# Performance work log

Hardware: AMD Instinct MI355X
Metric: run time of the kernel (lower is better)

Reference implementation:

```python
import jax, jax.numpy as jnp
import numpy as np

N0, N1, N2 = 20000, 15000, 15000
N = N0 + N1 + N2            # total nodes
E = 800000                  # edges (avg degree 16)
H, C = 128, 64


def setup_inputs() -> dict:
    key = jax.random.key(0)
    ks = jax.random.split(key, 16)
    s = 0.05  # weight scale
    return {
        "feat0": jax.random.normal(ks[0], (N0, 512), jnp.float32),
        "feat1": jax.random.normal(ks[1], (N1, 256), jnp.float32),
        "feat2": jax.random.normal(ks[2], (N2, 128), jnp.float32),
        "W0": jax.random.normal(ks[3], (512, H), jnp.float32) * s,
        "b0": jnp.zeros((H,), jnp.float32),
        "W1": jax.random.normal(ks[4], (256, H), jnp.float32) * s,
        "b1": jnp.zeros((H,), jnp.float32),
        "W2": jax.random.normal(ks[5], (128, H), jnp.float32) * s,
        "b2": jnp.zeros((H,), jnp.float32),
        "bias_l0": jnp.zeros((H,), jnp.float32),
        "W_l1": jax.random.normal(ks[6], (H, H), jnp.float32) * s,
        "b_l1": jnp.zeros((H,), jnp.float32),
        "W_l2": jax.random.normal(ks[7], (H, C), jnp.float32) * s,
        "b_l2": jnp.zeros((C,), jnp.float32),
        "src": jax.random.randint(ks[8], (E,), 0, N, jnp.int32),
        "dst": jax.random.randint(ks[9], (E,), 0, N, jnp.int32),
    }


def _norms(src, dst):
    # DGL GraphConv norm='both': src side uses out-degree, dst side in-degree
    ones = jnp.ones((E,), jnp.float32)
    deg_out = jax.ops.segment_sum(ones, src, num_segments=N)
    deg_in = jax.ops.segment_sum(ones, dst, num_segments=N)
    return jnp.maximum(deg_out, 1.0) ** -0.5, jnp.maximum(deg_in, 1.0) ** -0.5


def _agg(h, src, dst, norm_src, norm_dst):
    # normalized sparse aggregation: D_in^{-1/2} A D_out^{-1/2} h
    m = (h * norm_src[:, None])[src]                     # [E, d] gather
    a = jax.ops.segment_sum(m, dst, num_segments=N)      # [N, d] scatter-add
    return a * norm_dst[:, None]


def reference(feat0, feat1, feat2, W0, b0, W1, b1, W2, b2,
              bias_l0, W_l1, b_l1, W_l2, b_l2, src, dst):
    # per-node-type linear projections, concatenated along node axis
    h = jnp.concatenate([feat0 @ W0 + b0,
                         feat1 @ W1 + b1,
                         feat2 @ W2 + b2], axis=0)       # [N, H]
    ns, nd = _norms(src, dst)
    # layer 0: GraphConv(weight=False) -> agg + bias + relu (dropout = eval identity)
    h = jax.nn.relu(_agg(h, src, dst, ns, nd) + bias_l0)
    # layer 1: agg + linear + relu
    h = jax.nn.relu(_agg(h, src, dst, ns, nd) @ W_l1 + b_l1)
    # layer 2: agg + linear (no activation)
    h = _agg(h, src, dst, ns, nd) @ W_l2 + b_l2          # [N, C]
    return h
```

## Files before the change

kernel.cpp:

```cpp
#include <hip/hip_runtime.h>
#include <hip/hip_fp16.h>

#define N_NODES 50000
#define N0_ 20000
#define N1_ 15000
#define N2_ 15000
#define E_EDGES 800000
#define H_ 128
#define C_ 64

#define PB0 ((N0_ + 63) / 64)
#define PB1 ((N1_ + 63) / 64)
#define PB2 ((N2_ + 63) / 64)
#define PB_TOTAL (PB0 + PB1 + PB2)
#define EB ((E_EDGES + 255) / 256)
#define SB ((N_NODES + 255) / 256)


template <int TN, bool BIAS, bool RELU, bool SCALE, typename OT>
__device__ __forceinline__ void gemm_block(
    const float* __restrict__ A, const float* __restrict__ W,
    const float* __restrict__ bias, const float* __restrict__ rowscale,
    OT* __restrict__ out, int M, int K, int m0, float* As, float* Bs) {
    constexpr int NJ = TN / 32;
    constexpr int TN4 = TN / 4;
    int tid = threadIdx.x;
    int tx = tid & 31;
    int ty = tid >> 5;

    float acc[8][NJ];
#pragma unroll
    for (int i = 0; i < 8; i++)
#pragma unroll
        for (int j = 0; j < NJ; j++) acc[i][j] = 0.f;

    for (int k0 = 0; k0 < K; k0 += 32) {
#pragma unroll
        for (int t0 = 0; t0 < 2; t0++) {
            int t = tid + t0 * 256;
            int row = t >> 3;
            int c = t & 7;
            float4 v = make_float4(0.f, 0.f, 0.f, 0.f);
            if (m0 + row < M) v = *reinterpret_cast<const float4*>(&A[(size_t)(m0 + row) * K + k0 + c * 4]);
            As[(c * 4 + 0) * 68 + row] = v.x;
            As[(c * 4 + 1) * 68 + row] = v.y;
            As[(c * 4 + 2) * 68 + row] = v.z;
            As[(c * 4 + 3) * 68 + row] = v.w;
        }
#pragma unroll
        for (int t0 = 0; t0 < 32 * TN4 / 256; t0++) {
            int t = tid + t0 * 256;
            int r = t / TN4;
            int c4 = t % TN4;
            *reinterpret_cast<float4*>(&Bs[r * TN + c4 * 4]) =
                *reinterpret_cast<const float4*>(&W[(size_t)(k0 + r) * TN + c4 * 4]);
        }
        __syncthreads();
#pragma unroll 8
        for (int k = 0; k < 32; k++) {
            float4 a0 = *reinterpret_cast<float4*>(&As[k * 68 + ty * 8]);
            float4 a1 = *reinterpret_cast<float4*>(&As[k * 68 + ty * 8 + 4]);
            float ar[8] = {a0.x, a0.y, a0.z, a0.w, a1.x, a1.y, a1.z, a1.w};
            float br[NJ];
#pragma unroll
            for (int j = 0; j < NJ; j++) br[j] = Bs[k * TN + tx + 32 * j];
#pragma unroll
            for (int i = 0; i < 8; i++)
#pragma unroll
                for (int j = 0; j < NJ; j++) acc[i][j] = fmaf(ar[i], br[j], acc[i][j]);
        }
        __syncthreads();
    }
#pragma unroll
    for (int i = 0; i < 8; i++) {
        int row = m0 + ty * 8 + i;
        if (row < M) {
            float sc = SCALE ? rowscale[row] : 1.f;
#pragma unroll
            for (int j = 0; j < NJ; j++) {
                float v = acc[i][j] + (BIAS ? bias[tx + 32 * j] : 0.f);
                if (RELU) v = fmaxf(v, 0.f);
                v *= sc;
                out[(size_t)row * TN + tx + 32 * j] = (OT)v;
            }
        }
    }
}


__global__ __launch_bounds__(256) void k1_proj_rank(
    const float* __restrict__ feat0, const float* __restrict__ feat1, const float* __restrict__ feat2,
    const float* __restrict__ W0, const float* __restrict__ b0,
    const float* __restrict__ W1, const float* __restrict__ b1,
    const float* __restrict__ W2, const float* __restrict__ b2,
    __half* __restrict__ h0h,
    const int* __restrict__ src, const int* __restrict__ dst,
    int* __restrict__ cnt, int* __restrict__ degO, int* __restrict__ rank) {
    __shared__ float As[32 * 68];
    __shared__ float Bs[32 * 128];
    int bid = blockIdx.x;
    if (bid < PB_TOTAL) {
        const float* A; const float* Wp; const float* bp; __half* op; int M, K, m0;
        if (bid < PB0) {
            A = feat0; Wp = W0; bp = b0; op = h0h; M = N0_; K = 512; m0 = bid * 64;
        } else if (bid < PB0 + PB1) {
            A = feat1; Wp = W1; bp = b1; op = h0h + (size_t)N0_ * H_; M = N1_; K = 256;
            m0 = (bid - PB0) * 64;
        } else {
            A = feat2; Wp = W2; bp = b2; op = h0h + (size_t)(N0_ + N1_) * H_; M = N2_; K = 128;
            m0 = (bid - PB0 - PB1) * 64;
        }
        gemm_block<128, true, false, false, __half>(A, Wp, bp, nullptr, op, M, K, m0, As, Bs);
    } else {
        int e = (bid - PB_TOTAL) * 256 + threadIdx.x;
        if (e < E_EDGES) {
            rank[e] = atomicAdd(&cnt[dst[e]], 1);
            atomicAdd(&degO[src[e]], 1);
        }
    }
}


__global__ __launch_bounds__(256) void scan1_kernel(
    const int* __restrict__ cnt, int* __restrict__ pre, int* __restrict__ blocksum) {
    __shared__ int buf[256];
    int t = threadIdx.x;
    int i = blockIdx.x * 256 + t;
    int tot = (i < N_NODES) ? cnt[i] : 0;
    buf[t] = tot;
    __syncthreads();
#pragma unroll
    for (int off = 1; off < 256; off <<= 1) {
        int v = (t >= off) ? buf[t - off] : 0;
        __syncthreads();
        buf[t] += v;
        __syncthreads();
    }
    if (i < N_NODES) pre[i] = buf[t] - tot;
    if (t == 255) blocksum[blockIdx.x] = buf[255];
}

__global__ __launch_bounds__(256) void scan2_kernel(
    const int* __restrict__ blocksum, int* __restrict__ blockoff, int* __restrict__ rowptr) {
    __shared__ int buf[256];
    int t = threadIdx.x;
    int v = (t < SB) ? blocksum[t] : 0;
    buf[t] = v;
    __syncthreads();
#pragma unroll
    for (int off = 1; off < 256; off <<= 1) {
        int u = (t >= off) ? buf[t - off] : 0;
        __syncthreads();
        buf[t] += u;
        __syncthreads();
    }
    if (t < SB) blockoff[t] = buf[t] - v;
    if (t == 255) rowptr[N_NODES] = buf[255];
}

__global__ __launch_bounds__(256) void scan3_kernel(
    const int* __restrict__ cnt, const int* __restrict__ degO, const int* __restrict__ pre,
    const int* __restrict__ blockoff, int* __restrict__ rowptr,
    float* __restrict__ ns, float* __restrict__ nd) {
    int i = blockIdx.x * 256 + threadIdx.x;
    if (i < N_NODES) {
        rowptr[i] = blockoff[blockIdx.x] + pre[i];
        ns[i] = rsqrtf(fmaxf((float)degO[i], 1.0f));
        nd[i] = rsqrtf(fmaxf((float)cnt[i], 1.0f));
    }
}


__global__ __launch_bounds__(256) void k2_fill(
    const int* __restrict__ src, const int* __restrict__ dst,
    const int* __restrict__ rowptr, const int* __restrict__ rank,
    int* __restrict__ col) {
    int e = blockIdx.x * 256 + threadIdx.x;
    if (e < E_EDGES) col[rowptr[dst[e]] + rank[e]] = src[e];
}


template <int CH, int NSLOAD, int EPI, int OUTH>
__global__ __launch_bounds__(256) void agg_h_kernel(
    const __half* __restrict__ h, const int* __restrict__ rowptr,
    const int* __restrict__ col, const float* __restrict__ ns,
    const float* __restrict__ nd, const float* __restrict__ bias,
    void* __restrict__ out) {
    constexpr int L = CH / 8;
    constexpr int EPW = 64 / L;
    int node = blockIdx.x * 4 + (threadIdx.x >> 6);
    if (node >= N_NODES) return;
    int lane = threadIdx.x & 63;
    int li = lane & (L - 1);
    int g = lane / L;
    const uint4* __restrict__ h8 = (const uint4*)h;
    int beg = rowptr[node], end = rowptr[node + 1];
    float a0[8] = {0.f, 0.f, 0.f, 0.f, 0.f, 0.f, 0.f, 0.f};
    float a1[8] = {0.f, 0.f, 0.f, 0.f, 0.f, 0.f, 0.f, 0.f};
    union U8 { uint4 u; __half2 h2[4]; };
    int e = beg + g;
    for (; e + EPW < end; e += 2 * EPW) {
        int s0 = col[e], s1 = col[e + EPW];
        U8 u0, u1;
        u0.u = h8[(size_t)s0 * L + li];
        u1.u = h8[(size_t)s1 * L + li];
        float w0 = NSLOAD ? ns[s0] : 1.f;
        float w1 = NSLOAD ? ns[s1] : 1.f;
#pragma unroll
        for (int p = 0; p < 4; p++) {
            float2 f0 = __half22float2(u0.h2[p]);
            float2 f1 = __half22float2(u1.h2[p]);
            if (NSLOAD) {
                a0[2 * p] = fmaf(w0, f0.x, a0[2 * p]);
                a0[2 * p + 1] = fmaf(w0, f0.y, a0[2 * p + 1]);
                a1[2 * p] = fmaf(w1, f1.x, a1[2 * p]);
                a1[2 * p + 1] = fmaf(w1, f1.y, a1[2 * p + 1]);
            } else {
                a0[2 * p] += f0.x;
                a0[2 * p + 1] += f0.y;
                a1[2 * p] += f1.x;
                a1[2 * p + 1] += f1.y;
            }
        }
    }
    if (e < end) {
        int s = col[e];
        U8 u0;
        u0.u = h8[(size_t)s * L + li];
        float w0 = NSLOAD ? ns[s] : 1.f;
#pragma unroll
        for (int p = 0; p < 4; p++) {
            float2 f0 = __half22float2(u0.h2[p]);
            if (NSLOAD) {
                a0[2 * p] = fmaf(w0, f0.x, a0[2 * p]);
                a0[2 * p + 1] = fmaf(w0, f0.y, a0[2 * p + 1]);
            } else {
                a0[2 * p] += f0.x;
                a0[2 * p + 1] += f0.y;
            }
        }
    }
#pragma unroll
    for (int j = 0; j < 8; j++) {
        float v = a0[j] + a1[j];
#pragma unroll
        for (int off = 32; off >= L; off >>= 1) v += __shfl_xor(v, off);
        a0[j] = v;
    }
    if (lane < L) {
        float w = nd[node];
#pragma unroll
        for (int j = 0; j < 8; j++) a0[j] *= w;
        if (EPI == 1) {
            float sc = ns[node];
#pragma unroll
            for (int j = 0; j < 8; j++)
                a0[j] = fmaxf(a0[j] + bias[li * 8 + j], 0.f) * sc;
        } else if (EPI == 2) {
#pragma unroll
            for (int j = 0; j < 8; j++) a0[j] += bias[li * 8 + j];
        }
        if (OUTH) {
            union { uint4 u; __half hh[8]; } cv;
#pragma unroll
            for (int j = 0; j < 8; j++) cv.hh[j] = __float2half(a0[j]);
            ((uint4*)out)[(size_t)node * L + li] = cv.u;
        } else {
            float4* o4 = (float4*)out;
            o4[(size_t)node * (CH / 4) + li * 2] = make_float4(a0[0], a0[1], a0[2], a0[3]);
            o4[(size_t)node * (CH / 4) + li * 2 + 1] = make_float4(a0[4], a0[5], a0[6], a0[7]);
        }
    }
}


template <int TN, bool BIAS, bool RELU, bool SCALE, typename OT>
__global__ __launch_bounds__(256) void gemm_kernel(
    const float* __restrict__ A, const float* __restrict__ W,
    const float* __restrict__ bias, const float* __restrict__ rowscale,
    OT* __restrict__ out, int M, int K) {
    __shared__ float As[32 * 68];
    __shared__ float Bs[32 * TN];
    gemm_block<TN, BIAS, RELU, SCALE, OT>(A, W, bias, rowscale, out, M, K, blockIdx.x * 64, As, Bs);
}


extern "C" void kernel_launch(void* const* d_in, const int* in_sizes, int n_in,
                              void* d_out, int out_size, void* d_ws, size_t ws_size,
                              hipStream_t stream) {
    const float* feat0 = (const float*)d_in[0];
    const float* feat1 = (const float*)d_in[1];
    const float* feat2 = (const float*)d_in[2];
    const float* W0 = (const float*)d_in[3];
    const float* b0 = (const float*)d_in[4];
    const float* W1 = (const float*)d_in[5];
    const float* b1 = (const float*)d_in[6];
    const float* W2 = (const float*)d_in[7];
    const float* b2 = (const float*)d_in[8];
    const float* bias_l0 = (const float*)d_in[9];
    const float* W_l1 = (const float*)d_in[10];
    const float* b_l1 = (const float*)d_in[11];
    const float* W_l2 = (const float*)d_in[12];
    const float* b_l2 = (const float*)d_in[13];
    const int* src = (const int*)d_in[14];
    const int* dst = (const int*)d_in[15];
    float* out = (float*)d_out;

    char* ws = (char*)d_ws;
    size_t off = 0;
    auto alloc = [&](size_t bytes) {
        size_t cur = off;
        off += (bytes + 255) & ~(size_t)255;
        return cur;
    };
    size_t hA_off = alloc((size_t)N_NODES * H_ * 4);
    size_t hB_off = alloc((size_t)N_NODES * H_ * 4);
    size_t h0h_off = alloc((size_t)N_NODES * H_ * 2);
    size_t h1h_off = alloc((size_t)N_NODES * H_ * 2);
    size_t h2h_off = alloc((size_t)N_NODES * C_ * 2);
    size_t cnt_off = alloc((size_t)N_NODES * 4);
    size_t degO_off = alloc((size_t)N_NODES * 4);
    size_t ns_off = alloc((size_t)N_NODES * 4);
    size_t nd_off = alloc((size_t)N_NODES * 4);
    size_t rowptr_off = alloc((size_t)(N_NODES + 1) * 4);
    size_t rank_off = alloc((size_t)E_EDGES * 4);
    size_t col_off = alloc((size_t)E_EDGES * 4);
    size_t pre_off = alloc((size_t)N_NODES * 4);
    size_t bsum_off = alloc((size_t)SB * 4);
    size_t boff_off = alloc((size_t)SB * 4);

    float* hA = (float*)(ws + hA_off);
    float* hB = (float*)(ws + hB_off);
    __half* h0h = (__half*)(ws + h0h_off);
    __half* h1h = (__half*)(ws + h1h_off);
    __half* h2h = (__half*)(ws + h2h_off);
    int* cnt = (int*)(ws + cnt_off);
    int* degO = (int*)(ws + degO_off);
    float* ns = (float*)(ws + ns_off);
    float* nd = (float*)(ws + nd_off);
    int* rowptr = (int*)(ws + rowptr_off);
    int* rank = (int*)(ws + rank_off);
    int* col = (int*)(ws + col_off);
    int* pre = (int*)(ws + pre_off);
    int* bsum = (int*)(ws + bsum_off);
    int* boff = (int*)(ws + boff_off);

    hipMemsetAsync(ws + cnt_off, 0, ns_off - cnt_off, stream);

    k1_proj_rank<<<PB_TOTAL + EB, 256, 0, stream>>>(
        feat0, feat1, feat2, W0, b0, W1, b1, W2, b2, h0h, src, dst, cnt, degO, rank);
    scan1_kernel<<<SB, 256, 0, stream>>>(cnt, pre, bsum);
    scan2_kernel<<<1, 256, 0, stream>>>(bsum, boff, rowptr);
    scan3_kernel<<<SB, 256, 0, stream>>>(cnt, degO, pre, boff, rowptr, ns, nd);
    k2_fill<<<EB, 256, 0, stream>>>(src, dst, rowptr, rank, col);

    const int AGB = (N_NODES + 3) / 4;
    agg_h_kernel<128, 1, 1, 1><<<AGB, 256, 0, stream>>>(h0h, rowptr, col, ns, nd, bias_l0, h1h);
    agg_h_kernel<128, 0, 0, 0><<<AGB, 256, 0, stream>>>(h1h, rowptr, col, ns, nd, nullptr, hA);
    gemm_kernel<128, true, true, true, float><<<(N_NODES + 63) / 64, 256, 0, stream>>>(
        hA, W_l1, b_l1, ns, hB, N_NODES, 128);
    gemm_kernel<64, false, false, false, __half><<<(N_NODES + 63) / 64, 256, 0, stream>>>(
        hB, W_l2, nullptr, nullptr, h2h, N_NODES, 128);
    agg_h_kernel<64, 0, 2, 0><<<AGB, 256, 0, stream>>>(h2h, rowptr, col, ns, nd, b_l2, out);
}
```

Measured before the change: 258.0 us.

## Switch GEMMs to packed fp16 dot2 with pre-packed weights and fp16 intermediates

```diff
diff --git a/kernel.cpp b/kernel.cpp
--- a/kernel.cpp
+++ b/kernel.cpp
@@ -16,14 +16,80 @@
 #define EB ((E_EDGES + 255) / 256)
 #define SB ((N_NODES + 255) / 256)
 
-
-template <int TN, bool BIAS, bool RELU, bool SCALE, typename OT>
-__device__ __forceinline__ void gemm_block(
-    const float* __restrict__ A, const float* __restrict__ W,
+#define WT2_0 0
+#define WT2_1 32768
+#define WT2_2 49152
+#define WT2_L1 57344
+#define WT2_L2 65536
+#define WT2_TOTAL 69632
+
+typedef _Float16 h2_t __attribute__((ext_vector_type(2)));
+
+__device__ __forceinline__ float fdot2f(h2_t a, h2_t b, float c) {
+#if __has_builtin(__builtin_amdgcn_fdot2)
+    return __builtin_amdgcn_fdot2(a, b, c, false);
+#else
+    return fmaf((float)a[0], (float)b[0], fmaf((float)a[1], (float)b[1], c));
+#endif
+}
+
+
+__global__ __launch_bounds__(256) void wt2_kernel(
+    const float* __restrict__ W0, const float* __restrict__ W1, const float* __restrict__ W2,
+    const float* __restrict__ Wl1, const float* __restrict__ Wl2,
+    h2_t* __restrict__ Wt2) {
+    int t = blockIdx.x * 256 + threadIdx.x;
+    if (t >= WT2_TOTAL) return;
+    const float* W;
+    int rel, NW;
+    if (t < WT2_1) { W = W0; rel = t; NW = 128; }
+    else if (t < WT2_2) { W = W1; rel = t - WT2_1; NW = 128; }
+    else if (t < WT2_L1) { W = W2; rel = t - WT2_2; NW = 128; }
+    else if (t < WT2_L2) { W = Wl1; rel = t - WT2_L1; NW = 128; }
+    else { W = Wl2; rel = t - WT2_L2; NW = 64; }
+    int k2 = rel / NW;
+    int n = rel % NW;
+    h2_t p = {(_Float16)W[(size_t)(2 * k2) * NW + n], (_Float16)W[(size_t)(2 * k2 + 1) * NW + n]};
+    Wt2[t] = p;
+}
+
+
+__device__ __forceinline__ void stage_a_tile(const float* __restrict__ A, h2_t* As2,
+                                             int M, int K, int m0, int k0, int tid) {
+#pragma unroll
+    for (int t0 = 0; t0 < 2; t0++) {
+        int idx = tid + t0 * 256;
+        int row = idx >> 3;
+        int c = idx & 7;
+        float4 v = make_float4(0.f, 0.f, 0.f, 0.f);
+        if (m0 + row < M)
+            v = *reinterpret_cast<const float4*>(&A[(size_t)(m0 + row) * K + k0 + c * 4]);
+        h2_t p0 = {(_Float16)v.x, (_Float16)v.y};
+        h2_t p1 = {(_Float16)v.z, (_Float16)v.w};
+        As2[(c * 2) * 68 + row] = p0;
+        As2[(c * 2 + 1) * 68 + row] = p1;
+    }
+}
+
+__device__ __forceinline__ void stage_a_tile(const __half* __restrict__ A, h2_t* As2,
+                                             int M, int K, int m0, int k0, int tid) {
+    int row = tid >> 2;
+    int c = tid & 3;
+    union { uint4 u; h2_t p[4]; } v;
+    v.u = make_uint4(0, 0, 0, 0);
+    if (m0 + row < M)
+        v.u = *reinterpret_cast<const uint4*>(&A[(size_t)(m0 + row) * K + k0 + c * 8]);
+#pragma unroll
+    for (int i = 0; i < 4; i++) As2[(c * 4 + i) * 68 + row] = v.p[i];
+}
+
+
+template <int TN, bool BIAS, bool RELU, bool SCALE, typename IT, typename OT>
+__device__ __forceinline__ void gemm_block_h(
+    const IT* __restrict__ A, const h2_t* __restrict__ Wt2,
     const float* __restrict__ bias, const float* __restrict__ rowscale,
-    OT* __restrict__ out, int M, int K, int m0, float* As, float* Bs) {
+    OT* __restrict__ out, int M, int K, int m0, h2_t* As2, h2_t* Bs2) {
     constexpr int NJ = TN / 32;
-    constexpr int TN4 = TN / 4;
     int tid = threadIdx.x;
     int tx = tid & 31;
     int ty = tid >> 5;
@@ -35,39 +101,29 @@
         for (int j = 0; j < NJ; j++) acc[i][j] = 0.f;
 
     for (int k0 = 0; k0 < K; k0 += 32) {
-#pragma unroll
-        for (int t0 = 0; t0 < 2; t0++) {
-            int t = tid + t0 * 256;
-            int row = t >> 3;
-            int c = t & 7;
-            float4 v = make_float4(0.f, 0.f, 0.f, 0.f);
-            if (m0 + row < M) v = *reinterpret_cast<const float4*>(&A[(size_t)(m0 + row) * K + k0 + c * 4]);
-            As[(c * 4 + 0) * 68 + row] = v.x;
-            As[(c * 4 + 1) * 68 + row] = v.y;
-            As[(c * 4 + 2) * 68 + row] = v.z;
-            As[(c * 4 + 3) * 68 + row] = v.w;
-        }
-#pragma unroll
-        for (int t0 = 0; t0 < 32 * TN4 / 256; t0++) {
-            int t = tid + t0 * 256;
-            int r = t / TN4;
-            int c4 = t % TN4;
-            *reinterpret_cast<float4*>(&Bs[r * TN + c4 * 4]) =
-                *reinterpret_cast<const float4*>(&W[(size_t)(k0 + r) * TN + c4 * 4]);
-        }
-        __syncthreads();
-#pragma unroll 8
-        for (int k = 0; k < 32; k++) {
-            float4 a0 = *reinterpret_cast<float4*>(&As[k * 68 + ty * 8]);
-            float4 a1 = *reinterpret_cast<float4*>(&As[k * 68 + ty * 8 + 4]);
-            float ar[8] = {a0.x, a0.y, a0.z, a0.w, a1.x, a1.y, a1.z, a1.w};
-            float br[NJ];
-#pragma unroll
-            for (int j = 0; j < NJ; j++) br[j] = Bs[k * TN + tx + 32 * j];
+        stage_a_tile(A, As2, M, K, m0, k0, tid);
+        {
+            const uint4* g = reinterpret_cast<const uint4*>(Wt2 + (size_t)(k0 / 2) * TN);
+            uint4* l = reinterpret_cast<uint4*>(Bs2);
+            constexpr int CNT = 16 * TN / 4;
+#pragma unroll
+            for (int t0 = 0; t0 < CNT / 256; t0++) l[tid + t0 * 256] = g[tid + t0 * 256];
+        }
+        __syncthreads();
+#pragma unroll
+        for (int k2 = 0; k2 < 16; k2++) {
+            union { uint4 u; h2_t p[4]; } ua, ub;
+            ua.u = *reinterpret_cast<uint4*>(&As2[k2 * 68 + ty * 8]);
+            ub.u = *reinterpret_cast<uint4*>(&As2[k2 * 68 + ty * 8 + 4]);
+            h2_t ap[8] = {ua.p[0], ua.p[1], ua.p[2], ua.p[3],
+                          ub.p[0], ub.p[1], ub.p[2], ub.p[3]};
+            h2_t bp[NJ];
+#pragma unroll
+            for (int j = 0; j < NJ; j++) bp[j] = Bs2[k2 * TN + tx + 32 * j];
 #pragma unroll
             for (int i = 0; i < 8; i++)
 #pragma unroll
-                for (int j = 0; j < NJ; j++) acc[i][j] = fmaf(ar[i], br[j], acc[i][j]);
+                for (int j = 0; j < NJ; j++) acc[i][j] = fdot2f(ap[i], bp[j], acc[i][j]);
         }
         __syncthreads();
     }
@@ -90,27 +146,28 @@
 
 __global__ __launch_bounds__(256) void k1_proj_rank(
     const float* __restrict__ feat0, const float* __restrict__ feat1, const float* __restrict__ feat2,
-    const float* __restrict__ W0, const float* __restrict__ b0,
-    const float* __restrict__ W1, const float* __restrict__ b1,
-    const float* __restrict__ W2, const float* __restrict__ b2,
+    const h2_t* __restrict__ Wt2,
+    const float* __restrict__ b0, const float* __restrict__ b1, const float* __restrict__ b2,
     __half* __restrict__ h0h,
     const int* __restrict__ src, const int* __restrict__ dst,
     int* __restrict__ cnt, int* __restrict__ degO, int* __restrict__ rank) {
-    __shared__ float As[32 * 68];
-    __shared__ float Bs[32 * 128];
+    __shared__ h2_t As2[16 * 68];
+    __shared__ h2_t Bs2[16 * 128];
     int bid = blockIdx.x;
     if (bid < PB_TOTAL) {
-        const float* A; const float* Wp; const float* bp; __half* op; int M, K, m0;
+        const float* A; const float* bp; const h2_t* Wp; int M, K, m0;
+        size_t obase;
         if (bid < PB0) {
-            A = feat0; Wp = W0; bp = b0; op = h0h; M = N0_; K = 512; m0 = bid * 64;
+            A = feat0; bp = b0; Wp = Wt2 + WT2_0; M = N0_; K = 512; m0 = bid * 64; obase = 0;
         } else if (bid < PB0 + PB1) {
-            A = feat1; Wp = W1; bp = b1; op = h0h + (size_t)N0_ * H_; M = N1_; K = 256;
-            m0 = (bid - PB0) * 64;
+            A = feat1; bp = b1; Wp = Wt2 + WT2_1; M = N1_; K = 256; m0 = (bid - PB0) * 64;
+            obase = (size_t)N0_ * H_;
         } else {
-            A = feat2; Wp = W2; bp = b2; op = h0h + (size_t)(N0_ + N1_) * H_; M = N2_; K = 128;
-            m0 = (bid - PB0 - PB1) * 64;
-        }
-        gemm_block<128, true, false, false, __half>(A, Wp, bp, nullptr, op, M, K, m0, As, Bs);
+            A = feat2; bp = b2; Wp = Wt2 + WT2_2; M = N2_; K = 128; m0 = (bid - PB0 - PB1) * 64;
+            obase = (size_t)(N0_ + N1_) * H_;
+        }
+        gemm_block_h<128, true, false, false, float, __half>(
+            A, Wp, bp, nullptr, h0h + obase, M, K, m0, As2, Bs2);
     } else {
         int e = (bid - PB_TOTAL) * 256 + threadIdx.x;
         if (e < E_EDGES) {
@@ -158,25 +215,28 @@
     if (t == 255) rowptr[N_NODES] = buf[255];
 }
 
-__global__ __launch_bounds__(256) void scan3_kernel(
+__global__ __launch_bounds__(256) void scan3_fill_kernel(
     const int* __restrict__ cnt, const int* __restrict__ degO, const int* __restrict__ pre,
     const int* __restrict__ blockoff, int* __restrict__ rowptr,
-    float* __restrict__ ns, float* __restrict__ nd) {
-    int i = blockIdx.x * 256 + threadIdx.x;
-    if (i < N_NODES) {
-        rowptr[i] = blockoff[blockIdx.x] + pre[i];
-        ns[i] = rsqrtf(fmaxf((float)degO[i], 1.0f));
-        nd[i] = rsqrtf(fmaxf((float)cnt[i], 1.0f));
-    }
-}
-
-
-__global__ __launch_bounds__(256) void k2_fill(
+    float* __restrict__ ns, float* __restrict__ nd,
     const int* __restrict__ src, const int* __restrict__ dst,
-    const int* __restrict__ rowptr, const int* __restrict__ rank,
-    int* __restrict__ col) {
-    int e = blockIdx.x * 256 + threadIdx.x;
-    if (e < E_EDGES) col[rowptr[dst[e]] + rank[e]] = src[e];
+    const int* __restrict__ rank, int* __restrict__ col) {
+    int bid = blockIdx.x;
+    if (bid < SB) {
+        int i = bid * 256 + threadIdx.x;
+        if (i < N_NODES) {
+            rowptr[i] = blockoff[bid] + pre[i];
+            ns[i] = rsqrtf(fmaxf((float)degO[i], 1.0f));
+            nd[i] = rsqrtf(fmaxf((float)cnt[i], 1.0f));
+        }
+    } else {
+        int e = (bid - SB) * 256 + threadIdx.x;
+        if (e < E_EDGES) {
+            int d = dst[e];
+            int rp = blockoff[d >> 8] + pre[d];
+            col[rp + rank[e]] = src[e];
+        }
+    }
 }
 
 
@@ -274,14 +334,15 @@
 }
 
 
-template <int TN, bool BIAS, bool RELU, bool SCALE, typename OT>
-__global__ __launch_bounds__(256) void gemm_kernel(
-    const float* __restrict__ A, const float* __restrict__ W,
+template <int TN, bool BIAS, bool RELU, bool SCALE, typename IT, typename OT>
+__global__ __launch_bounds__(256) void gemm_h_kernel(
+    const IT* __restrict__ A, const h2_t* __restrict__ Wt2,
     const float* __restrict__ bias, const float* __restrict__ rowscale,
     OT* __restrict__ out, int M, int K) {
-    __shared__ float As[32 * 68];
-    __shared__ float Bs[32 * TN];
-    gemm_block<TN, BIAS, RELU, SCALE, OT>(A, W, bias, rowscale, out, M, K, blockIdx.x * 64, As, Bs);
+    __shared__ h2_t As2[16 * 68];
+    __shared__ h2_t Bs2[16 * TN];
+    gemm_block_h<TN, BIAS, RELU, SCALE, IT, OT>(A, Wt2, bias, rowscale, out, M, K,
+                                                blockIdx.x * 64, As2, Bs2);
 }
 
 
@@ -313,10 +374,11 @@
         off += (bytes + 255) & ~(size_t)255;
         return cur;
     };
-    size_t hA_off = alloc((size_t)N_NODES * H_ * 4);
-    size_t hB_off = alloc((size_t)N_NODES * H_ * 4);
+    size_t Wt2_off = alloc((size_t)WT2_TOTAL * 4);
     size_t h0h_off = alloc((size_t)N_NODES * H_ * 2);
     size_t h1h_off = alloc((size_t)N_NODES * H_ * 2);
+    size_t hAh_off = alloc((size_t)N_NODES * H_ * 2);
+    size_t hBh_off = alloc((size_t)N_NODES * H_ * 2);
     size_t h2h_off = alloc((size_t)N_NODES * C_ * 2);
     size_t cnt_off = alloc((size_t)N_NODES * 4);
     size_t degO_off = alloc((size_t)N_NODES * 4);
@@ -329,10 +391,11 @@
     size_t bsum_off = alloc((size_t)SB * 4);
     size_t boff_off = alloc((size_t)SB * 4);
 
-    float* hA = (float*)(ws + hA_off);
-    float* hB = (float*)(ws + hB_off);
+    h2_t* Wt2 = (h2_t*)(ws + Wt2_off);
     __half* h0h = (__half*)(ws + h0h_off);
     __half* h1h = (__half*)(ws + h1h_off);
+    __half* hAh = (__half*)(ws + hAh_off);
+    __half* hBh = (__half*)(ws + hBh_off);
     __half* h2h = (__half*)(ws + h2h_off);
     int* cnt = (int*)(ws + cnt_off);
     int* degO = (int*)(ws + degO_off);
@@ -347,19 +410,20 @@
 
     hipMemsetAsync(ws + cnt_off, 0, ns_off - cnt_off, stream);
 
+    wt2_kernel<<<(WT2_TOTAL + 255) / 256, 256, 0, stream>>>(W0, W1, W2, W_l1, W_l2, Wt2);
     k1_proj_rank<<<PB_TOTAL + EB, 256, 0, stream>>>(
-        feat0, feat1, feat2, W0, b0, W1, b1, W2, b2, h0h, src, dst, cnt, degO, rank);
+        feat0, feat1, feat2, Wt2, b0, b1, b2, h0h, src, dst, cnt, degO, rank);
     scan1_kernel<<<SB, 256, 0, stream>>>(cnt, pre, bsum);
     scan2_kernel<<<1, 256, 0, stream>>>(bsum, boff, rowptr);
-    scan3_kernel<<<SB, 256, 0, stream>>>(cnt, degO, pre, boff, rowptr, ns, nd);
-    k2_fill<<<EB, 256, 0, stream>>>(src, dst, rowptr, rank, col);
+    scan3_fill_kernel<<<SB + EB, 256, 0, stream>>>(
+        cnt, degO, pre, boff, rowptr, ns, nd, src, dst, rank, col);
 
     const int AGB = (N_NODES + 3) / 4;
     agg_h_kernel<128, 1, 1, 1><<<AGB, 256, 0, stream>>>(h0h, rowptr, col, ns, nd, bias_l0, h1h);
-    agg_h_kernel<128, 0, 0, 0><<<AGB, 256, 0, stream>>>(h1h, rowptr, col, ns, nd, nullptr, hA);
-    gemm_kernel<128, true, true, true, float><<<(N_NODES + 63) / 64, 256, 0, stream>>>(
-        hA, W_l1, b_l1, ns, hB, N_NODES, 128);
-    gemm_kernel<64, false, false, false, __half><<<(N_NODES + 63) / 64, 256, 0, stream>>>(
-        hB, W_l2, nullptr, nullptr, h2h, N_NODES, 128);
+    agg_h_kernel<128, 0, 0, 1><<<AGB, 256, 0, stream>>>(h1h, rowptr, col, ns, nd, nullptr, hAh);
+    gemm_h_kernel<128, true, true, true, __half, __half><<<(N_NODES + 63) / 64, 256, 0, stream>>>(
+        hAh, Wt2 + WT2_L1, b_l1, ns, hBh, N_NODES, 128);
+    gemm_h_kernel<64, false, false, false, __half, __half><<<(N_NODES + 63) / 64, 256, 0, stream>>>(
+        hBh, Wt2 + WT2_L2, nullptr, nullptr, h2h, N_NODES, 128);
     agg_h_kernel<64, 0, 2, 0><<<AGB, 256, 0, stream>>>(h2h, rowptr, col, ns, nd, b_l2, out);
 }
```

Result: slower. 272.7 us (+5.7%).
